# Performance work log

Measured on AMD Instinct MI355X. Metric: run time of the kernel, lower is better.

## Reference

```python
import jax, jax.numpy as jnp
import numpy as np

MUL = 128                  # multiplicity of each irrep slot in in1 / out
Z = 100000                 # batch (e.g. number of edges)
L = [0, 1]                 # l of irrep slot i; dims are 2l+1 -> [1, 3]
INSTR = [(0, 0, 0), (0, 1, 1), (1, 0, 1), (1, 1, 0)]  # parity-allowed 'uvw' paths


def _w3j_np(l1, l2, l3):
    """Real-basis Wigner-3j (e3nn convention) for l <= 1."""
    if (l1, l2, l3) == (0, 0, 0):
        return np.ones((1, 1, 1))
    e = np.eye(3) / np.sqrt(3.0)
    if (l1, l2, l3) == (1, 1, 0):
        return e[:, :, None]
    if (l1, l2, l3) == (0, 1, 1):
        return e[None, :, :]
    if (l1, l2, l3) == (1, 0, 1):
        return e[:, None, :]
    raise ValueError((l1, l2, l3))


# fan-in per output slot for component-normalized path weights
FAN_IN = {0: 0, 1: 0}
for (_i1, _i2, _io) in INSTR:
    FAN_IN[_io] += MUL * 1  # mul_in1 * mul_in2 for 'uvw'

WEIGHT_NUMEL = len(INSTR) * MUL * 1 * MUL  # 65536


def setup_inputs() -> dict:
    key = jax.random.key(0)
    k1, k2, k3 = jax.random.split(key, 3)
    x1 = jax.random.normal(k1, (Z, MUL * 1 + MUL * 3), jnp.float32)   # 128x0e + 128x1o
    x2 = jax.random.normal(k2, (Z, 1 + 3), jnp.float32)               # 1x0e + 1x1o
    weights = jax.random.normal(k3, (WEIGHT_NUMEL,), jnp.float32)     # shared 'uvw' weights
    return {"x1": x1, "x2": x2, "weights": weights}


def _tensor_product(x1, x2, weights):
    z = x1.shape[0]
    # split flat features into (mul, 2l+1) segments
    x1s = [x1[:, :MUL].reshape(z, MUL, 1), x1[:, MUL:].reshape(z, MUL, 3)]
    x2s = [x2[:, :1].reshape(z, 1, 1), x2[:, 1:].reshape(z, 1, 3)]
    outs = [jnp.zeros((z, MUL, 1), x1.dtype), jnp.zeros((z, MUL, 3), x1.dtype)]
    off = 0
    for (i1, i2, io) in INSTR:
        nw = MUL * 1 * MUL
        w = weights[off:off + nw].reshape(MUL, 1, MUL)  # (u, v, w)
        off += nw
        C = jnp.asarray(_w3j_np(L[i1], L[i2], L[io]), x1.dtype)
        pw = jnp.asarray(np.sqrt(2 * L[io] + 1.0) / np.sqrt(FAN_IN[io]), x1.dtype)
        # segmented CG contraction: small (i,j,k) dims, large z,u,w dims
        tmp = jnp.einsum('zui,zvj,ijk->zuvk', x1s[i1], x2s[i2], C)
        outs[io] = outs[io] + pw * jnp.einsum('zuvk,uvw->zwk', tmp, w)
    return jnp.concatenate([o.reshape(z, -1) for o in outs], axis=1)


def reference(x1, x2, weights):
    return _tensor_product(x1, x2, weights)
```

## Files before the change

### kernel.cpp

```cpp
#include <hip/hip_runtime.h>


#define Z_TOTAL   100000
#define BM        32
#define NTILES_Z  (Z_TOTAL / BM)
#define GRID      512
#define THREADS   512

using bf16x8 = __attribute__((ext_vector_type(8))) __bf16;
using f32x4  = __attribute__((ext_vector_type(4))) float;
using u16x8  = __attribute__((ext_vector_type(8))) unsigned short;

__device__ __forceinline__ unsigned short f2bf(float f) {
    unsigned int u = __builtin_bit_cast(unsigned int, f);
    u += 0x7fffu + ((u >> 16) & 1u);
    return (unsigned short)(u >> 16);
}

__device__ __forceinline__ int lds_idx(int row, int chunk) {
    return row * 256 + ((chunk ^ (row & 7)) << 3);
}

__global__ __launch_bounds__(THREADS, 4)
void tp_kernel(const float* __restrict__ x1, const float* __restrict__ x2,
               const float* __restrict__ wts, float* __restrict__ out)
{
    __shared__ __align__(16) unsigned short lds[128 * 256];

    const int t    = threadIdx.x;
    const int lane = t & 63;
    const int wv   = t >> 6;
    const int m16  = lane & 15;
    const int q    = lane >> 4;

    const float S16 = 0.0625f;
    const float S48 = 0.0625f * 0.57735026918962576f;
    bf16x8 Bf[2][8];
    {
        const int n = wv * 16 + m16;
        #pragma unroll
        for (int mat = 0; mat < 2; ++mat) {
            #pragma unroll
            for (int kt = 0; kt < 8; ++kt) {
                u16x8 bb;
                #pragma unroll
                for (int j = 0; j < 8; ++j) {
                    const int k = kt * 32 + q * 8 + j;
                    float v;
                    if (mat == 0) {
                        v = (k < 128) ? wts[k * 128 + n] * S16
                                      : wts[49152 + (k - 128) * 128 + n] * S48;
                    } else {
                        v = (k < 128) ? wts[16384 + k * 128 + n] * S16
                                      : wts[32768 + (k - 128) * 128 + n] * S16;
                    }
                    bb[j] = f2bf(v);
                }
                Bf[mat][kt] = __builtin_bit_cast(bf16x8, bb);
            }
        }
    }

    const int zl = t >> 4;
    const int ug = t & 15;
    const int u0 = ug * 8;

    for (int tile = blockIdx.x; tile < NTILES_Z; tile += gridDim.x) {
        const int z0 = tile * BM;
        const float* xr = x1 + (size_t)(z0 + zl) * 512;

        __syncthreads();
        {
            const float4 b4 = *(const float4*)(x2 + (size_t)(z0 + zl) * 4);
            const float b0 = b4.x, b1x = b4.y, b1y = b4.z, b1z = b4.w;

            const float4 a0a = *(const float4*)(xr + u0);
            const float4 a0b = *(const float4*)(xr + u0 + 4);
            const float a0[8] = {a0a.x, a0a.y, a0a.z, a0a.w,
                                 a0b.x, a0b.y, a0b.z, a0b.w};
            u16x8 pk;
            #pragma unroll
            for (int i = 0; i < 8; ++i) pk[i] = f2bf(b0 * a0[i]);
            *(u16x8*)&lds[lds_idx(zl, ug)] = pk;
            #pragma unroll
            for (int i = 0; i < 8; ++i) pk[i] = f2bf(b1x * a0[i]);
            *(u16x8*)&lds[lds_idx(32 + zl, ug)] = pk;
            #pragma unroll
            for (int i = 0; i < 8; ++i) pk[i] = f2bf(b1y * a0[i]);
            *(u16x8*)&lds[lds_idx(64 + zl, ug)] = pk;
            #pragma unroll
            for (int i = 0; i < 8; ++i) pk[i] = f2bf(b1z * a0[i]);
            *(u16x8*)&lds[lds_idx(96 + zl, ug)] = pk;

            float a1[24];
            #pragma unroll
            for (int i = 0; i < 6; ++i) {
                const float4 v = *(const float4*)(xr + 128 + u0 * 3 + i * 4);
                a1[i*4+0] = v.x; a1[i*4+1] = v.y; a1[i*4+2] = v.z; a1[i*4+3] = v.w;
            }
            #pragma unroll
            for (int i = 0; i < 8; ++i)
                pk[i] = f2bf(a1[3*i]*b1x + a1[3*i+1]*b1y + a1[3*i+2]*b1z);
            *(u16x8*)&lds[lds_idx(zl, 16 + ug)] = pk;
            #pragma unroll
            for (int i = 0; i < 8; ++i) pk[i] = f2bf(b0 * a1[3*i + 0]);
            *(u16x8*)&lds[lds_idx(32 + zl, 16 + ug)] = pk;
            #pragma unroll
            for (int i = 0; i < 8; ++i) pk[i] = f2bf(b0 * a1[3*i + 1]);
            *(u16x8*)&lds[lds_idx(64 + zl, 16 + ug)] = pk;
            #pragma unroll
            for (int i = 0; i < 8; ++i) pk[i] = f2bf(b0 * a1[3*i + 2]);
            *(u16x8*)&lds[lds_idx(96 + zl, 16 + ug)] = pk;
        }
        __syncthreads();

        const int n = wv * 16 + m16;
        #pragma unroll
        for (int mt = 0; mt < 8; ++mt) {
            const int isV1 = (mt >= 2) ? 1 : 0;
            const int k3 = isV1 ? ((mt - 2) >> 1) : 0;
            const int zt = isV1 ? ((mt - 2) & 1) : 0;
            const int rbase = isV1 ? (32 + k3 * 32 + zt * 16) : (mt * 16);
            const int r = rbase + m16;
            f32x4 acc = {0.f, 0.f, 0.f, 0.f};
            #pragma unroll
            for (int kt = 0; kt < 8; ++kt) {
                const bf16x8 a = __builtin_bit_cast(bf16x8,
                    *(const u16x8*)&lds[lds_idx(r, kt * 4 + q)]);
                acc = __builtin_amdgcn_mfma_f32_16x16x32_bf16(a, Bf[isV1][kt], acc, 0, 0, 0);
            }
            if (!isV1) {
                #pragma unroll
                for (int reg = 0; reg < 4; ++reg) {
                    const int z = z0 + mt * 16 + q * 4 + reg;
                    out[(size_t)z * 512 + n] = acc[reg];
                }
            } else {
                #pragma unroll
                for (int reg = 0; reg < 4; ++reg) {
                    const int z = z0 + zt * 16 + q * 4 + reg;
                    out[(size_t)z * 512 + 128 + n * 3 + k3] = acc[reg];
                }
            }
        }
    }
}

extern "C" void kernel_launch(void* const* d_in, const int* in_sizes, int n_in,
                              void* d_out, int out_size, void* d_ws, size_t ws_size,
                              hipStream_t stream) {
    (void)in_sizes; (void)n_in; (void)d_ws; (void)ws_size; (void)out_size;
    const float* x1  = (const float*)d_in[0];
    const float* x2  = (const float*)d_in[1];
    const float* wts = (const float*)d_in[2];
    float* out = (float*)d_out;
    tp_kernel<<<dim3(GRID), dim3(THREADS), 0, stream>>>(x1, x2, wts, out);
}
```

Measured before the change: 380.4 us.

## Prefetch next tile into registers during MFMA and vectorize l=1 output stores

Restructures the persistent tile loop so global loads for the next tile are issued into a second register set while the current tile's MFMAs and stores run, hiding memory latency. Also groups the three k3 accumulators so each output row writes a packed 3-float struct instead of scattered scalar stores, uses nontemporal stores for the scalar output, and switches to native bf16 conversion. Costs extra registers for the double-buffered tile data, which may pressure occupancy under the 4-block launch bound.

```diff
diff --git a/kernel.cpp b/kernel.cpp
--- a/kernel.cpp
+++ b/kernel.cpp
@@ -9,16 +9,110 @@
 
 using bf16x8 = __attribute__((ext_vector_type(8))) __bf16;
 using f32x4  = __attribute__((ext_vector_type(4))) float;
-using u16x8  = __attribute__((ext_vector_type(8))) unsigned short;
 
-__device__ __forceinline__ unsigned short f2bf(float f) {
-    unsigned int u = __builtin_bit_cast(unsigned int, f);
-    u += 0x7fffu + ((u >> 16) & 1u);
-    return (unsigned short)(u >> 16);
-}
+struct __align__(4) F3 { float x, y, z; };
+
+struct TileRegs {
+    float4 b;
+    float4 a0a, a0b;
+    float4 a1[6];
+};
 
 __device__ __forceinline__ int lds_idx(int row, int chunk) {
     return row * 256 + ((chunk ^ (row & 7)) << 3);
+}
+
+__device__ __forceinline__ void tile_load(TileRegs& T, const float* __restrict__ x1,
+                                          const float* __restrict__ x2,
+                                          int z0, int zl, int u0) {
+    const float* xr = x1 + (size_t)(z0 + zl) * 512;
+    T.b   = *(const float4*)(x2 + (size_t)(z0 + zl) * 4);
+    T.a0a = *(const float4*)(xr + u0);
+    T.a0b = *(const float4*)(xr + u0 + 4);
+    #pragma unroll
+    for (int i = 0; i < 6; ++i)
+        T.a1[i] = *(const float4*)(xr + 128 + u0 * 3 + i * 4);
+}
+
+__device__ __forceinline__ void tile_stage(const TileRegs& T, unsigned short* lds,
+                                           int zl, int ug) {
+    const float b0 = T.b.x, b1x = T.b.y, b1y = T.b.z, b1z = T.b.w;
+    const float a0[8] = {T.a0a.x, T.a0a.y, T.a0a.z, T.a0a.w,
+                         T.a0b.x, T.a0b.y, T.a0b.z, T.a0b.w};
+    bf16x8 pk;
+    #pragma unroll
+    for (int i = 0; i < 8; ++i) pk[i] = (__bf16)(b0 * a0[i]);
+    *(bf16x8*)&lds[lds_idx(zl, ug)] = pk;
+    #pragma unroll
+    for (int i = 0; i < 8; ++i) pk[i] = (__bf16)(b1x * a0[i]);
+    *(bf16x8*)&lds[lds_idx(32 + zl, ug)] = pk;
+    #pragma unroll
+    for (int i = 0; i < 8; ++i) pk[i] = (__bf16)(b1y * a0[i]);
+    *(bf16x8*)&lds[lds_idx(64 + zl, ug)] = pk;
+    #pragma unroll
+    for (int i = 0; i < 8; ++i) pk[i] = (__bf16)(b1z * a0[i]);
+    *(bf16x8*)&lds[lds_idx(96 + zl, ug)] = pk;
+
+    float a1[24];
+    #pragma unroll
+    for (int i = 0; i < 6; ++i) {
+        a1[i*4+0] = T.a1[i].x; a1[i*4+1] = T.a1[i].y;
+        a1[i*4+2] = T.a1[i].z; a1[i*4+3] = T.a1[i].w;
+    }
+    #pragma unroll
+    for (int i = 0; i < 8; ++i)
+        pk[i] = (__bf16)(a1[3*i]*b1x + a1[3*i+1]*b1y + a1[3*i+2]*b1z);
+    *(bf16x8*)&lds[lds_idx(zl, 16 + ug)] = pk;
+    #pragma unroll
+    for (int i = 0; i < 8; ++i) pk[i] = (__bf16)(b0 * a1[3*i + 0]);
+    *(bf16x8*)&lds[lds_idx(32 + zl, 16 + ug)] = pk;
+    #pragma unroll
+    for (int i = 0; i < 8; ++i) pk[i] = (__bf16)(b0 * a1[3*i + 1]);
+    *(bf16x8*)&lds[lds_idx(64 + zl, 16 + ug)] = pk;
+    #pragma unroll
+    for (int i = 0; i < 8; ++i) pk[i] = (__bf16)(b0 * a1[3*i + 2]);
+    *(bf16x8*)&lds[lds_idx(96 + zl, 16 + ug)] = pk;
+}
+
+__device__ __forceinline__ void mfma_store(const unsigned short* lds,
+                                           const bf16x8 Bf[2][8],
+                                           float* __restrict__ out,
+                                           int z0, int m16, int q, int n) {
+    #pragma unroll
+    for (int m2 = 0; m2 < 2; ++m2) {
+        f32x4 acc = {0.f, 0.f, 0.f, 0.f};
+        const int r = m2 * 16 + m16;
+        #pragma unroll
+        for (int kt = 0; kt < 8; ++kt) {
+            const bf16x8 a = *(const bf16x8*)&lds[lds_idx(r, kt * 4 + q)];
+            acc = __builtin_amdgcn_mfma_f32_16x16x32_bf16(a, Bf[0][kt], acc, 0, 0, 0);
+        }
+        #pragma unroll
+        for (int reg = 0; reg < 4; ++reg) {
+            const int z = z0 + m2 * 16 + q * 4 + reg;
+            __builtin_nontemporal_store(acc[reg], out + (size_t)z * 512 + n);
+        }
+    }
+    #pragma unroll
+    for (int zt = 0; zt < 2; ++zt) {
+        f32x4 a3[3];
+        #pragma unroll
+        for (int k3 = 0; k3 < 3; ++k3) {
+            a3[k3] = (f32x4){0.f, 0.f, 0.f, 0.f};
+            const int r = 32 + k3 * 32 + zt * 16 + m16;
+            #pragma unroll
+            for (int kt = 0; kt < 8; ++kt) {
+                const bf16x8 a = *(const bf16x8*)&lds[lds_idx(r, kt * 4 + q)];
+                a3[k3] = __builtin_amdgcn_mfma_f32_16x16x32_bf16(a, Bf[1][kt], a3[k3], 0, 0, 0);
+            }
+        }
+        #pragma unroll
+        for (int reg = 0; reg < 4; ++reg) {
+            const int z = z0 + zt * 16 + q * 4 + reg;
+            F3 v; v.x = a3[0][reg]; v.y = a3[1][reg]; v.z = a3[2][reg];
+            *(F3*)(out + (size_t)z * 512 + 128 + n * 3) = v;
+        }
+    }
 }
 
 __global__ __launch_bounds__(THREADS, 4)
@@ -42,7 +136,7 @@
         for (int mat = 0; mat < 2; ++mat) {
             #pragma unroll
             for (int kt = 0; kt < 8; ++kt) {
-                u16x8 bb;
+                bf16x8 bb;
                 #pragma unroll
                 for (int j = 0; j < 8; ++j) {
                     const int k = kt * 32 + q * 8 + j;
@@ -54,9 +148,9 @@
                         v = (k < 128) ? wts[16384 + k * 128 + n] * S16
                                       : wts[32768 + (k - 128) * 128 + n] * S16;
                     }
-                    bb[j] = f2bf(v);
+                    bb[j] = (__bf16)v;
                 }
-                Bf[mat][kt] = __builtin_bit_cast(bf16x8, bb);
+                Bf[mat][kt] = bb;
             }
         }
     }
@@ -64,85 +158,32 @@
     const int zl = t >> 4;
     const int ug = t & 15;
     const int u0 = ug * 8;
+    const int n  = wv * 16 + m16;
 
-    for (int tile = blockIdx.x; tile < NTILES_Z; tile += gridDim.x) {
-        const int z0 = tile * BM;
-        const float* xr = x1 + (size_t)(z0 + zl) * 512;
+    int tile = blockIdx.x;
+    TileRegs P, N;
+    tile_load(P, x1, x2, tile * BM, zl, u0);
 
+    for (;;) {
+        int nx = tile + GRID;
         __syncthreads();
-        {
-            const float4 b4 = *(const float4*)(x2 + (size_t)(z0 + zl) * 4);
-            const float b0 = b4.x, b1x = b4.y, b1y = b4.z, b1z = b4.w;
+        tile_stage(P, lds, zl, ug);
+        __syncthreads();
+        if (nx < NTILES_Z)
+            tile_load(N, x1, x2, nx * BM, zl, u0);
+        mfma_store(lds, Bf, out, tile * BM, m16, q, n);
+        if (nx >= NTILES_Z) return;
+        tile = nx;
 
-            const float4 a0a = *(const float4*)(xr + u0);
-            const float4 a0b = *(const float4*)(xr + u0 + 4);
-            const float a0[8] = {a0a.x, a0a.y, a0a.z, a0a.w,
-                                 a0b.x, a0b.y, a0b.z, a0b.w};
-            u16x8 pk;
-            #pragma unroll
-            for (int i = 0; i < 8; ++i) pk[i] = f2bf(b0 * a0[i]);
-            *(u16x8*)&lds[lds_idx(zl, ug)] = pk;
-            #pragma unroll
-            for (int i = 0; i < 8; ++i) pk[i] = f2bf(b1x * a0[i]);
-            *(u16x8*)&lds[lds_idx(32 + zl, ug)] = pk;
-            #pragma unroll
-            for (int i = 0; i < 8; ++i) pk[i] = f2bf(b1y * a0[i]);
-            *(u16x8*)&lds[lds_idx(64 + zl, ug)] = pk;
-            #pragma unroll
-            for (int i = 0; i < 8; ++i) pk[i] = f2bf(b1z * a0[i]);
-            *(u16x8*)&lds[lds_idx(96 + zl, ug)] = pk;
-
-            float a1[24];
-            #pragma unroll
-            for (int i = 0; i < 6; ++i) {
-                const float4 v = *(const float4*)(xr + 128 + u0 * 3 + i * 4);
-                a1[i*4+0] = v.x; a1[i*4+1] = v.y; a1[i*4+2] = v.z; a1[i*4+3] = v.w;
-            }
-            #pragma unroll
-            for (int i = 0; i < 8; ++i)
-                pk[i] = f2bf(a1[3*i]*b1x + a1[3*i+1]*b1y + a1[3*i+2]*b1z);
-            *(u16x8*)&lds[lds_idx(zl, 16 + ug)] = pk;
-            #pragma unroll
-            for (int i = 0; i < 8; ++i) pk[i] = f2bf(b0 * a1[3*i + 0]);
-            *(u16x8*)&lds[lds_idx(32 + zl, 16 + ug)] = pk;
-            #pragma unroll
-            for (int i = 0; i < 8; ++i) pk[i] = f2bf(b0 * a1[3*i + 1]);
-            *(u16x8*)&lds[lds_idx(64 + zl, 16 + ug)] = pk;
-            #pragma unroll
-            for (int i = 0; i < 8; ++i) pk[i] = f2bf(b0 * a1[3*i + 2]);
-            *(u16x8*)&lds[lds_idx(96 + zl, 16 + ug)] = pk;
-        }
+        nx = tile + GRID;
         __syncthreads();
-
-        const int n = wv * 16 + m16;
-        #pragma unroll
-        for (int mt = 0; mt < 8; ++mt) {
-            const int isV1 = (mt >= 2) ? 1 : 0;
-            const int k3 = isV1 ? ((mt - 2) >> 1) : 0;
-            const int zt = isV1 ? ((mt - 2) & 1) : 0;
-            const int rbase = isV1 ? (32 + k3 * 32 + zt * 16) : (mt * 16);
-            const int r = rbase + m16;
-            f32x4 acc = {0.f, 0.f, 0.f, 0.f};
-            #pragma unroll
-            for (int kt = 0; kt < 8; ++kt) {
-                const bf16x8 a = __builtin_bit_cast(bf16x8,
-                    *(const u16x8*)&lds[lds_idx(r, kt * 4 + q)]);
-                acc = __builtin_amdgcn_mfma_f32_16x16x32_bf16(a, Bf[isV1][kt], acc, 0, 0, 0);
-            }
-            if (!isV1) {
-                #pragma unroll
-                for (int reg = 0; reg < 4; ++reg) {
-                    const int z = z0 + mt * 16 + q * 4 + reg;
-                    out[(size_t)z * 512 + n] = acc[reg];
-                }
-            } else {
-                #pragma unroll
-                for (int reg = 0; reg < 4; ++reg) {
-                    const int z = z0 + zt * 16 + q * 4 + reg;
-                    out[(size_t)z * 512 + 128 + n * 3 + k3] = acc[reg];
-                }
-            }
-        }
+        tile_stage(N, lds, zl, ug);
+        __syncthreads();
+        if (nx < NTILES_Z)
+            tile_load(P, x1, x2, nx * BM, zl, u0);
+        mfma_store(lds, Bf, out, tile * BM, m16, q, n);
+        if (nx >= NTILES_Z) return;
+        tile = nx;
     }
 }
 
```

Result: slower. 508.5 us (+33.7%).
